# Kernel tuning notes

Hardware: AMD Instinct MI355X
Metric: run time of the kernel (lower is better)

Reference implementation:

```python
import jax, jax.numpy as jnp
import numpy as np

B = 4            # batch size (coords[:,0].max()+1 in the original)
C = 64           # NUM_BEV_FEATURES
NX, NY, NZ = 432, 496, 1
P_PER = 16000    # pillars per sample per bin
N_BINS = 3       # intersweep_sequence_length


def _make_coords(seed):
    # unique BEV cells per sample: strided modular arange (stride coprime with NX*NY)
    stride = 9973
    cells = (np.arange(P_PER, dtype=np.int64)[None, :] * stride + 17 * seed + 31 * np.arange(B)[:, None]) % (NX * NY)
    y = (cells // NX).reshape(-1)
    x = (cells % NX).reshape(-1)
    b = np.repeat(np.arange(B, dtype=np.int64), P_PER)
    z = np.zeros_like(b)
    return jnp.asarray(np.stack([b, z, y, x], axis=1), dtype=jnp.int32)  # [B*P_PER, 4]


def setup_inputs() -> dict:
    key = jax.random.key(0)
    inp = {}
    for i in range(N_BINS):
        key, kf = jax.random.split(key)
        inp[f"pillar_features_bin_{i}"] = jax.random.normal(kf, (B * P_PER, C), dtype=jnp.float32)
        inp[f"voxel_coords_bin_{i}"] = _make_coords(i)
    return inp


def _scatter_bin(pillars, coords):
    # coords layout: [batch, z, y, x]; per-sample flat index = z + y*nx + x (nz==1)
    c = coords.astype(jnp.int32)
    flat = c[:, 0] * (NY * NX) + c[:, 1] + c[:, 2] * NX + c[:, 3]  # batch-offset flattened index
    canvas = jnp.zeros((B * NY * NX, C), dtype=pillars.dtype).at[flat].set(pillars)
    return canvas.reshape(B, NY, NX, C).transpose(0, 3, 1, 2)  # [B, C, NY, NX]


def reference(pillar_features_bin_0, voxel_coords_bin_0,
              pillar_features_bin_1, voxel_coords_bin_1,
              pillar_features_bin_2, voxel_coords_bin_2):
    out0 = _scatter_bin(pillar_features_bin_0, voxel_coords_bin_0)
    out1 = _scatter_bin(pillar_features_bin_1, voxel_coords_bin_1)
    out2 = _scatter_bin(pillar_features_bin_2, voxel_coords_bin_2)
    return (out0, out1, out2)
```

## Files before the change

kernel.cpp:

```cpp
#include <hip/hip_runtime.h>

#define NX_ 432
#define NY_ 496
#define C_  64
#define B_  4
#define CELLS_ (NX_ * NY_)
#define PLANE_ ((size_t)CELLS_)
#define BATCH_STRIDE_ ((size_t)C_ * CELLS_)
#define BIN_STRIDE_   ((size_t)B_ * C_ * CELLS_)
#define MAP_BIN_ ((size_t)B_ * CELLS_)

typedef float vfloat4 __attribute__((ext_vector_type(4)));
typedef int   vint4   __attribute__((ext_vector_type(4)));

__global__ __launch_bounds__(256) void scatter_idx_kernel(
    const int* __restrict__ coords0,
    const int* __restrict__ coords1,
    const int* __restrict__ coords2,
    int* __restrict__ map, int npil)
{
    const int bin = blockIdx.y;
    const int p = blockIdx.x * 256 + threadIdx.x;
    if (p >= npil) return;
    const int* coords = (bin == 0) ? coords0 : (bin == 1) ? coords1 : coords2;
    vint4 c = ((const vint4*)coords)[p];
    size_t idx = (size_t)bin * MAP_BIN_ + (size_t)c.x * CELLS_ + c.y + c.z * NX_ + c.w;
    map[idx] = p;
}

__global__ __launch_bounds__(256) void gather_kernel(
    const float* __restrict__ pf0,
    const float* __restrict__ pf1,
    const float* __restrict__ pf2,
    const int* __restrict__ map,
    float* __restrict__ out)
{
    const int bin = blockIdx.z;
    const int b   = blockIdx.y;
    const int cell = blockIdx.x * 1024 + threadIdx.x * 4;
    if (cell >= CELLS_) return;

    const float* __restrict__ pf = (bin == 0) ? pf0 : (bin == 1) ? pf1 : pf2;

    const int* m = map + (size_t)bin * MAP_BIN_ + (size_t)b * CELLS_ + cell;
    vint4 idx = *(const vint4*)m;

    const bool v0 = idx.x >= 0, v1 = idx.y >= 0, v2 = idx.z >= 0, v3 = idx.w >= 0;
    const float* r0 = pf + (size_t)(v0 ? idx.x : 0) * C_;
    const float* r1 = pf + (size_t)(v1 ? idx.y : 0) * C_;
    const float* r2 = pf + (size_t)(v2 ? idx.z : 0) * C_;
    const float* r3 = pf + (size_t)(v3 ? idx.w : 0) * C_;

    float* o = out + (size_t)bin * BIN_STRIDE_ + (size_t)b * BATCH_STRIDE_ + cell;

#pragma unroll 4
    for (int c = 0; c < C_; ++c) {
        float x0 = r0[c];
        float x1 = r1[c];
        float x2 = r2[c];
        float x3 = r3[c];
        vfloat4 v;
        v.x = v0 ? x0 : 0.0f;
        v.y = v1 ? x1 : 0.0f;
        v.z = v2 ? x2 : 0.0f;
        v.w = v3 ? x3 : 0.0f;
        __builtin_nontemporal_store(v, (vfloat4*)(o + (size_t)c * PLANE_));
    }
}

extern "C" void kernel_launch(void* const* d_in, const int* in_sizes, int n_in,
                              void* d_out, int out_size, void* d_ws, size_t ws_size,
                              hipStream_t stream) {
    const float* pf0 = (const float*)d_in[0];
    const int*   co0 = (const int*)d_in[1];
    const float* pf1 = (const float*)d_in[2];
    const int*   co1 = (const int*)d_in[3];
    const float* pf2 = (const float*)d_in[4];
    const int*   co2 = (const int*)d_in[5];
    float* out = (float*)d_out;

    const int npil = in_sizes[1] / 4;

    int* map = (int*)d_ws;
    const size_t map_bytes = 3 * MAP_BIN_ * sizeof(int);

    (void)hipMemsetAsync(map, 0xFF, map_bytes, stream);

    dim3 g1((npil + 255) / 256, 3, 1);
    scatter_idx_kernel<<<g1, 256, 0, stream>>>(co0, co1, co2, map, npil);

    dim3 g2((CELLS_ + 1023) / 1024, B_, 3);
    gather_kernel<<<g2, 256, 0, stream>>>(pf0, pf1, pf2, map, out);
}
```

Measured before the change: 701.6 us.

## Gather 8 cells per thread with float4 row loads and software prefetch

Each gather thread now handles 8 output cells instead of 4. It loads pillar feature rows as float4 vectors instead of scalars, and prefetches the next 4-channel group while storing the current one. It also writes 32 bytes per channel plane per thread and sets an occupancy hint through launch_bounds. This aims to cut load instruction count and hide gather latency, at the cost of more registers and fewer threads in flight.

```diff
diff --git a/kernel.cpp b/kernel.cpp
--- a/kernel.cpp
+++ b/kernel.cpp
@@ -28,7 +28,7 @@
     map[idx] = p;
 }
 
-__global__ __launch_bounds__(256) void gather_kernel(
+__global__ __launch_bounds__(256, 4) void gather_kernel(
     const float* __restrict__ pf0,
     const float* __restrict__ pf1,
     const float* __restrict__ pf2,
@@ -37,34 +37,58 @@
 {
     const int bin = blockIdx.z;
     const int b   = blockIdx.y;
-    const int cell = blockIdx.x * 1024 + threadIdx.x * 4;
+    const int cell = (blockIdx.x * 256 + threadIdx.x) * 8;
     if (cell >= CELLS_) return;
 
     const float* __restrict__ pf = (bin == 0) ? pf0 : (bin == 1) ? pf1 : pf2;
 
     const int* m = map + (size_t)bin * MAP_BIN_ + (size_t)b * CELLS_ + cell;
-    vint4 idx = *(const vint4*)m;
+    vint4 ia = ((const vint4*)m)[0];
+    vint4 ib = ((const vint4*)m)[1];
 
-    const bool v0 = idx.x >= 0, v1 = idx.y >= 0, v2 = idx.z >= 0, v3 = idx.w >= 0;
-    const float* r0 = pf + (size_t)(v0 ? idx.x : 0) * C_;
-    const float* r1 = pf + (size_t)(v1 ? idx.y : 0) * C_;
-    const float* r2 = pf + (size_t)(v2 ? idx.z : 0) * C_;
-    const float* r3 = pf + (size_t)(v3 ? idx.w : 0) * C_;
+    const int id[8] = { ia.x, ia.y, ia.z, ia.w, ib.x, ib.y, ib.z, ib.w };
+    bool v[8];
+    const float* r[8];
+#pragma unroll
+    for (int j = 0; j < 8; ++j) {
+        v[j] = id[j] >= 0;
+        r[j] = pf + (size_t)(v[j] ? id[j] : 0) * C_;
+    }
 
     float* o = out + (size_t)bin * BIN_STRIDE_ + (size_t)b * BATCH_STRIDE_ + cell;
 
-#pragma unroll 4
-    for (int c = 0; c < C_; ++c) {
-        float x0 = r0[c];
-        float x1 = r1[c];
-        float x2 = r2[c];
-        float x3 = r3[c];
-        vfloat4 v;
-        v.x = v0 ? x0 : 0.0f;
-        v.y = v1 ? x1 : 0.0f;
-        v.z = v2 ? x2 : 0.0f;
-        v.w = v3 ? x3 : 0.0f;
-        __builtin_nontemporal_store(v, (vfloat4*)(o + (size_t)c * PLANE_));
+    vfloat4 cur[8], nxt[8];
+#pragma unroll
+    for (int j = 0; j < 8; ++j)
+        cur[j] = *(const vfloat4*)(r[j]);
+
+#pragma unroll
+    for (int g = 0; g < 16; ++g) {
+        if (g < 15) {
+#pragma unroll
+            for (int j = 0; j < 8; ++j)
+                nxt[j] = *(const vfloat4*)(r[j] + (g + 1) * 4);
+        }
+#pragma unroll
+        for (int q = 0; q < 4; ++q) {
+            vfloat4 w0, w1;
+            w0.x = v[0] ? cur[0][q] : 0.0f;
+            w0.y = v[1] ? cur[1][q] : 0.0f;
+            w0.z = v[2] ? cur[2][q] : 0.0f;
+            w0.w = v[3] ? cur[3][q] : 0.0f;
+            w1.x = v[4] ? cur[4][q] : 0.0f;
+            w1.y = v[5] ? cur[5][q] : 0.0f;
+            w1.z = v[6] ? cur[6][q] : 0.0f;
+            w1.w = v[7] ? cur[7][q] : 0.0f;
+            float* po = o + (size_t)(4 * g + q) * PLANE_;
+            __builtin_nontemporal_store(w0, (vfloat4*)(po));
+            __builtin_nontemporal_store(w1, (vfloat4*)(po + 4));
+        }
+        if (g < 15) {
+#pragma unroll
+            for (int j = 0; j < 8; ++j)
+                cur[j] = nxt[j];
+        }
     }
 }
 
@@ -89,6 +113,6 @@
     dim3 g1((npil + 255) / 256, 3, 1);
     scatter_idx_kernel<<<g1, 256, 0, stream>>>(co0, co1, co2, map, npil);
 
-    dim3 g2((CELLS_ + 1023) / 1024, B_, 3);
+    dim3 g2((CELLS_ / 8 + 255) / 256, B_, 3);
     gather_kernel<<<g2, 256, 0, stream>>>(pf0, pf1, pf2, map, out);
 }
```

Result: slower. 932.8 us (+33.0%).
